# Performance work log

Hardware: AMD Instinct MI355X
Metric: run time of the kernel (lower is better)

## Reference

```python
import math
import jax, jax.numpy as jnp
import numpy as np

E = 1024      # embed_dim
K = 512       # key_dim
H = 16        # num_heads
W = 32        # scale window length (scale_lengths[0])
LENGTHS = [640, 512, 768, 384, 512, 576, 448, 256]
T = sum(LENGTHS)   # 4096 flat tokens
B = len(LENGTHS)
MAXL = max(LENGTHS)


def setup_inputs() -> dict:
    key = jax.random.key(0)
    ks = jax.random.split(key, 6)
    s = 0.02
    x = jax.random.normal(ks[0], (T, E), jnp.float32)
    Wkv = jax.random.normal(ks[1], (E + K, E), jnp.float32) * s
    bkv = jnp.zeros((E + K,), jnp.float32)
    Wq = jax.random.normal(ks[2], (K, E), jnp.float32) * s
    bq = jnp.zeros((K,), jnp.float32)
    Wp = jax.random.normal(ks[3], (E, E), jnp.float32) * s
    bp = jnp.zeros((E,), jnp.float32)
    # reset_parameters: init.uniform_ on layer buffer
    buffer = jax.random.uniform(ks[4], (W - 1, E + K), jnp.float32)
    sample_lengths = jnp.array(LENGTHS, jnp.int32)
    return {"x": x, "Wkv": Wkv, "bkv": bkv, "Wq": Wq, "bq": bq,
            "Wp": Wp, "bp": bp, "buffer": buffer,
            "sample_lengths": sample_lengths}


def reference(x, Wkv, bkv, Wq, bq, Wp, bp, buffer, sample_lengths):
    Tn, En = x.shape
    # per-token segment id and local position within the sample
    starts = jnp.concatenate([jnp.zeros((1,), sample_lengths.dtype),
                              jnp.cumsum(sample_lengths)[:-1]])
    t = jnp.arange(Tn, dtype=starts.dtype)
    seg = jnp.searchsorted(starts, t, side='right') - 1   # [T]
    j = t - starts[seg]                                   # local index in sample

    # key_value projection on the flat batch
    kv = x @ Wkv.T + bkv                                  # [T, E+K]

    # tile_within: window[c] = token(j - c) within sample, else learned buffer pad
    # (matches roll_by_gather semantics: window order is self, prev1, prev2, ...)
    c = jnp.arange(W)
    src = jnp.concatenate([buffer, kv], axis=0)           # [W-1 + T, E+K]
    data_idx = (W - 1) + t[:, None] - c[None, :]          # global token j - c
    buf_idx = (W - 1) + j[:, None] - c[None, :]           # buffer[W-1 + (j-c)]
    idx = jnp.where(j[:, None] >= c[None, :], data_idx, buf_idx)
    tiled = src[idx]                                      # [T, W, E+K]

    dk = K // H
    dv = En // H
    kh = tiled[..., :K].reshape(Tn, W, H, dk)
    vh = tiled[..., K:].reshape(Tn, W, H, dv)
    q = (x @ Wq.T + bq).reshape(Tn, H, dk)

    # single-query scaled dot-product attention over the W-window
    logits = jnp.einsum('thd,twhd->thw', q, kh) * (1.0 / math.sqrt(dk))
    p = jax.nn.softmax(logits, axis=-1)                   # [T, H, W]
    o = jnp.einsum('thw,twhd->thd', p, vh).reshape(Tn, En)
    out = o @ Wp.T + bp                                   # [T, E]

    # unflatten (pack/pad_sequence): scatter flat tokens into padded [B, MAXL, E]
    y = jnp.zeros((B, MAXL, En), out.dtype).at[seg, j].set(out)
    return y
```

## Files before the change

kernel.cpp:

```cpp
#include <hip/hip_runtime.h>

typedef __attribute__((ext_vector_type(8))) short short8v;
typedef __attribute__((ext_vector_type(4))) float f32x4;

__device__ inline unsigned short f2b(float f) {
    unsigned u = __builtin_bit_cast(unsigned, f);
    unsigned r = u + 0x7fffu + ((u >> 16) & 1u);
    return (unsigned short)(r >> 16);
}
__device__ inline void gload16(const void* g, void* l) {
    __builtin_amdgcn_global_load_lds(
        (const __attribute__((address_space(1))) void*)g,
        (__attribute__((address_space(3))) void*)l, 16, 0, 0);
}

__global__ __launch_bounds__(256)
void prep_kernel(const float* __restrict__ x, const float* __restrict__ wkv,
                 const float* __restrict__ wq, const float* __restrict__ wp,
                 const float* __restrict__ buf, const int* __restrict__ sl,
                 const float* __restrict__ bkv, const float* __restrict__ bq,
                 short* __restrict__ dst, short* __restrict__ ext,
                 int* __restrict__ extrow, int* __restrict__ destrow,
                 float* __restrict__ biascat,
                 long n0, long n1, long n2, long n3, long n4,
                 int T, int Bn, int MAXL, int EK, int NKVQ)
{
    long gid = (long)blockIdx.x * blockDim.x + threadIdx.x;
    long e = gid * 8;
    if (e < n3) {
        const float* s; long off;
        if (e < n0)      { s = x;   off = e; }
        else if (e < n1) { s = wkv; off = e - n0; }
        else if (e < n2) { s = wq;  off = e - n1; }
        else             { s = wp;  off = e - n2; }
        float4 a = *(const float4*)(s + off);
        float4 b = *(const float4*)(s + off + 4);
        short8v o;
        o[0] = (short)f2b(a.x); o[1] = (short)f2b(a.y);
        o[2] = (short)f2b(a.z); o[3] = (short)f2b(a.w);
        o[4] = (short)f2b(b.x); o[5] = (short)f2b(b.y);
        o[6] = (short)f2b(b.z); o[7] = (short)f2b(b.w);
        *(short8v*)(dst + e) = o;
    } else if (e < n4) {
        long off = e - n3;
        int brow = (int)(off / EK);
        int bcol = (int)(off % EK);
        float4 a = *(const float4*)(buf + off);
        float4 b = *(const float4*)(buf + off + 4);
        short8v o;
        o[0] = (short)f2b(a.x); o[1] = (short)f2b(a.y);
        o[2] = (short)f2b(a.z); o[3] = (short)f2b(a.w);
        o[4] = (short)f2b(b.x); o[5] = (short)f2b(b.y);
        o[6] = (short)f2b(b.z); o[7] = (short)f2b(b.w);
        int start = 0;
        for (int s = 0; s < 8; ++s) {
            int dr = 31 * s + start + brow;
            *(short8v*)&ext[(size_t)dr * EK + bcol] = o;
            start += sl[s];
        }
    }
    if (gid < T) {
        int start = 0, seg = 0, jloc = 0;
        for (int i = 0; i < Bn; ++i) {
            int len = sl[i];
            if (gid >= start && gid < start + len) { seg = i; jloc = (int)gid - start; }
            start += len;
        }
        destrow[gid] = seg * MAXL + jloc;
        extrow[gid]  = 31 * (seg + 1) + (int)gid;
    }
    if (gid < NKVQ) {
        biascat[gid] = (gid < EK) ? bkv[gid] : bq[gid - EK];
    }
}

__global__ __launch_bounds__(256)
void padzero_kernel(float* __restrict__ y, const int* __restrict__ sl,
                    int MAXL, int E)
{
    int row = blockIdx.x;
    int seg = row / MAXL, pos = row - seg * MAXL;
    if (pos < sl[seg]) return;
    float4 z = {0.f, 0.f, 0.f, 0.f};
    *(float4*)&y[(size_t)row * E + threadIdx.x * 4] = z;
}

template<int MODE>
__global__ __launch_bounds__(512)
void gemm8w(const short* __restrict__ A, const short* __restrict__ Bm,
            const float* __restrict__ bias,
            short* __restrict__ C0, short* __restrict__ C1,
            float* __restrict__ Cf, const int* __restrict__ rowmap,
            int M, int N, int Kd)
{
    __shared__ short lA[2][128 * 64];
    __shared__ short lB[2][128 * 64];
    int nb = N >> 7;
    int bid0 = blockIdx.x;
    int bid = (bid0 & 7) * ((int)gridDim.x >> 3) + (bid0 >> 3);
    int m0 = (bid / nb) << 7, n0 = (bid % nb) << 7;
    int tid = threadIdx.x;
    int lane = tid & 63, wid = tid >> 6;
    int wm = wid >> 1, wn = wid & 1;
    int nlo = lane & 15, g4 = lane >> 4;

    f32x4 acc[2][4];
    #pragma unroll
    for (int i = 0; i < 2; ++i)
        #pragma unroll
        for (int j2 = 0; j2 < 4; ++j2)
            acc[i][j2] = (f32x4)(0.f);

    int srow = tid >> 3;
    int scol = (tid & 7) * 8;
    const short* ga = A + (size_t)(m0 + srow) * Kd + scol;
    const short* gb = Bm + (size_t)(n0 + srow) * Kd + scol;

    auto stage = [&](int bf2, int k0) {
        gload16(ga + k0,                   &lA[bf2][srow * 64 + scol]);
        gload16(ga + (size_t)64 * Kd + k0, &lA[bf2][(64 + srow) * 64 + scol]);
        gload16(gb + k0,                   &lB[bf2][srow * 64 + scol]);
        gload16(gb + (size_t)64 * Kd + k0, &lB[bf2][(64 + srow) * 64 + scol]);
    };

    int nk = Kd >> 6;
    stage(0, 0);
    for (int t = 0; t < nk; ++t) {
        __syncthreads();
        if (t + 1 < nk) stage((t + 1) & 1, (t + 1) << 6);
        int cb = t & 1;
        #pragma unroll
        for (int ss = 0; ss < 2; ++ss) {
            short8v af[2], bf[4];
            #pragma unroll
            for (int f = 0; f < 2; ++f)
                af[f] = *(const short8v*)
                    &lA[cb][(wm * 32 + f * 16 + nlo) * 64 + ss * 32 + g4 * 8];
            #pragma unroll
            for (int f = 0; f < 4; ++f)
                bf[f] = *(const short8v*)
                    &lB[cb][(wn * 64 + f * 16 + nlo) * 64 + ss * 32 + g4 * 8];
            #pragma unroll
            for (int i = 0; i < 2; ++i)
                #pragma unroll
                for (int j2 = 0; j2 < 4; ++j2)
                    acc[i][j2] = __builtin_amdgcn_mfma_f32_16x16x32_bf16(
                        af[i], bf[j2], acc[i][j2], 0, 0, 0);
        }
    }

    int cr = g4 * 4;
    float bv[4];
    #pragma unroll
    for (int j2 = 0; j2 < 4; ++j2)
        bv[j2] = bias[n0 + wn * 64 + j2 * 16 + nlo];
    #pragma unroll
    for (int i = 0; i < 2; ++i) {
        #pragma unroll
        for (int rr = 0; rr < 4; ++rr) {
            int row = m0 + wm * 32 + i * 16 + cr + rr;
            int dr = rowmap[row];
            #pragma unroll
            for (int j2 = 0; j2 < 4; ++j2) {
                int col = n0 + wn * 64 + j2 * 16 + nlo;
                float v = acc[i][j2][rr] + bv[j2];
                if (MODE == 0) {
                    if (col < 1536)
                        C0[(size_t)dr * 1536 + col] = (short)f2b(v);
                    else
                        C1[(size_t)row * 512 + (col - 1536)] = (short)f2b(v);
                } else {
                    Cf[(size_t)dr * N + col] = v;
                }
            }
        }
    }
}

__global__ __launch_bounds__(256)
void attn6_kernel(const short* __restrict__ ext, const short* __restrict__ qb,
                  const int* __restrict__ extrow, short* __restrict__ o)
{
    __shared__ short lK[4 * 48 * 40];
    __shared__ short lV[4 * 48 * 66];
    __shared__ short ps[4 * 16 * 76];

    int bid = blockIdx.x;
    int swz = (bid & 7) * (gridDim.x >> 3) + (bid >> 3);
    int tg = swz >> 2, hg = swz & 3;
    int t0 = tg << 4, h0 = hg << 2;
    int r0 = extrow[t0] - 31;
    int tid = threadIdx.x;
    int wv = tid >> 6, lane = tid & 63;

    #pragma unroll
    for (int p = 0; p < 3; ++p) {
        int q = p * 256 + tid;
        int hd = q / 192;
        int rem = q - hd * 192;
        int rr = rem >> 2, cc = rem & 3;
        int sr = r0 + (rr < 47 ? rr : 46);
        *(short8v*)&lK[hd * 1920 + rr * 40 + cc * 8] =
            *(const short8v*)&ext[(size_t)sr * 1536 + (h0 + hd) * 32 + cc * 8];
    }
    #pragma unroll
    for (int p = 0; p < 6; ++p) {
        int q = p * 256 + tid;
        int hd = q / 384;
        int rem = q - hd * 384;
        int rr = rem >> 3, cc = rem & 7;
        int sr = r0 + (rr < 47 ? rr : 46);
        *(short8v*)&lV[hd * 3168 + rr * 66 + cc * 8] =
            *(const short8v*)&ext[(size_t)sr * 1536 + 512 + (h0 + hd) * 64 + cc * 8];
    }
    if (tid < 128) {
        int hd = tid >> 5, row = (tid >> 1) & 15, hf = tid & 1;
        uint4 z = {0u, 0u, 0u, 0u};
        *(uint4*)&ps[hd * 1216 + row * 76 + 48 + hf * 8] = z;
    }

    int h = h0 + wv;
    int nlo = lane & 15, g4 = lane >> 4;

    short8v aq = *(const short8v*)&qb[(size_t)(t0 + nlo) * 512 + h * 32 + g4 * 8];

    __syncthreads();

    f32x4 sg[3];
    #pragma unroll
    for (int g = 0; g < 3; ++g) {
        short8v bk = *(const short8v*)&lK[wv * 1920 + (g * 16 + nlo) * 40 + g4 * 8];
        f32x4 z = (f32x4)(0.f);
        sg[g] = __builtin_amdgcn_mfma_f32_16x16x32_bf16(aq, bk, z, 0, 0, 0);
    }

    const float scale = 0.17677669529663687f;
    #pragma unroll
    for (int r = 0; r < 4; ++r) {
        int tk = g4 * 4 + r;
        bool v0 = (nlo >= tk);
        bool v2 = (nlo < tk);
        float s0 = v0 ? sg[0][r] * scale : -1e30f;
        float s1 = sg[1][r] * scale;
        float s2 = v2 ? sg[2][r] * scale : -1e30f;
        float m = fmaxf(fmaxf(s0, s1), s2);
        m = fmaxf(m, __shfl_xor(m, 1, 64));
        m = fmaxf(m, __shfl_xor(m, 2, 64));
        m = fmaxf(m, __shfl_xor(m, 4, 64));
        m = fmaxf(m, __shfl_xor(m, 8, 64));
        float p0 = v0 ? __expf(s0 - m) : 0.f;
        float p1 = __expf(s1 - m);
        float p2 = v2 ? __expf(s2 - m) : 0.f;
        float sm = p0 + p1 + p2;
        sm += __shfl_xor(sm, 1, 64);
        sm += __shfl_xor(sm, 2, 64);
        sm += __shfl_xor(sm, 4, 64);
        sm += __shfl_xor(sm, 8, 64);
        float inv = 1.f / sm;
        short* pr = &ps[wv * 1216 + tk * 76];
        pr[nlo]      = (short)f2b(p0 * inv);
        pr[16 + nlo] = (short)f2b(p1 * inv);
        pr[32 + nlo] = (short)f2b(p2 * inv);
    }

    short8v pa0 = *(const short8v*)&ps[wv * 1216 + nlo * 76 + g4 * 8];
    short8v pa1 = *(const short8v*)&ps[wv * 1216 + nlo * 76 + 32 + g4 * 8];
    #pragma unroll
    for (int dvt = 0; dvt < 4; ++dvt) {
        f32x4 acc = (f32x4)(0.f);
        short8v b0, b1;
        #pragma unroll
        for (int j = 0; j < 8; ++j) {
            int lr = g4 * 8 + j;
            b0[j] = lV[wv * 3168 + lr * 66 + dvt * 16 + nlo];
        }
        acc = __builtin_amdgcn_mfma_f32_16x16x32_bf16(pa0, b0, acc, 0, 0, 0);
        #pragma unroll
        for (int j = 0; j < 8; ++j) {
            int lr = 32 + g4 * 8 + j;
            int rowc = lr < 47 ? lr : 47;
            b1[j] = lV[wv * 3168 + rowc * 66 + dvt * 16 + nlo];
        }
        acc = __builtin_amdgcn_mfma_f32_16x16x32_bf16(pa1, b1, acc, 0, 0, 0);
        #pragma unroll
        for (int r = 0; r < 4; ++r) {
            int t = t0 + g4 * 4 + r;
            o[(size_t)t * 1024 + h * 64 + dvt * 16 + nlo] = (short)f2b(acc[r]);
        }
    }
}

extern "C" void kernel_launch(void* const* d_in, const int* in_sizes, int n_in,
                              void* d_out, int out_size, void* d_ws, size_t ws_size,
                              hipStream_t stream)
{
    const float* x      = (const float*)d_in[0];
    const float* Wkv    = (const float*)d_in[1];
    const float* bkv    = (const float*)d_in[2];
    const float* Wq     = (const float*)d_in[3];
    const float* bq     = (const float*)d_in[4];
    const float* Wp     = (const float*)d_in[5];
    const float* bp     = (const float*)d_in[6];
    const float* buffer = (const float*)d_in[7];
    const int*   sl     = (const int*)d_in[8];

    int E  = in_sizes[6];
    int Kc = in_sizes[4];
    int T  = in_sizes[0] / E;
    int Bn = in_sizes[8];
    int EK = E + Kc;
    int NKVQ = EK + Kc;
    int MAXL = out_size / (Bn * E);
    int TEXT = T + 31 * Bn;

    size_t nX = (size_t)T * E, nWkv = (size_t)EK * E, nWq = (size_t)Kc * E;
    size_t nWp = (size_t)E * E, nBuf = (size_t)in_sizes[7];

    short* xb    = (short*)d_ws;
    short* wkvqb = xb + nX;
    short* wpb   = wkvqb + nWkv + nWq;
    short* qbuf  = wpb + nWp;
    short* extb  = qbuf + (size_t)T * Kc;
    short* ob    = extb + (size_t)TEXT * EK;
    int*   extrowp = (int*)(ob + (size_t)T * E);
    int*   destrow = extrowp + T;
    float* biascat = (float*)(destrow + T);

    float* y = (float*)d_out;

    long n0 = (long)nX, n1 = n0 + (long)nWkv, n2 = n1 + (long)nWq;
    long n3 = n2 + (long)nWp, n4 = n3 + (long)nBuf;
    int prep_blocks = (int)((n4 / 8 + 255) / 256);
    prep_kernel<<<prep_blocks, 256, 0, stream>>>(
        x, Wkv, Wq, Wp, buffer, sl, bkv, bq, xb, extb,
        extrowp, destrow, biascat,
        n0, n1, n2, n3, n4, T, Bn, MAXL, EK, NKVQ);

    padzero_kernel<<<Bn * MAXL, E / 4, 0, stream>>>(y, sl, MAXL, E);

    gemm8w<0><<<(T / 128) * (NKVQ / 128), 512, 0, stream>>>(
        xb, wkvqb, biascat, extb, qbuf, nullptr, extrowp, T, NKVQ, E);

    attn6_kernel<<<(T / 16) * 4, 256, 0, stream>>>(extb, qbuf, extrowp, ob);

    gemm8w<1><<<(T / 128) * (E / 128), 512, 0, stream>>>(
        ob, wpb, bp, nullptr, nullptr, y, destrow, T, E, E);
}
```

Baseline: 82.69 us.

## Fuse all stages into one persistent kernel with grid-wide barriers

Replaces the five separate launches (prep, pad-zero, QKV GEMM, window attention, output GEMM) with a single persistent kernel of 512 blocks of 256 threads. The stages are separated by an atomic grid barrier, and each block loops over several work tiles. GEMM tiles are re-shaped to K-step 32, and each block handles two attention tiles. The aim is to remove launch gaps and tail effects between kernels. In exchange it depends on all 512 blocks being co-resident, adds barrier spin cost, and lowers per-block thread counts for the GEMMs.

```diff
diff --git a/kernel.cpp b/kernel.cpp
--- a/kernel.cpp
+++ b/kernel.cpp
@@ -14,278 +14,324 @@
         (__attribute__((address_space(3))) void*)l, 16, 0, 0);
 }
 
-__global__ __launch_bounds__(256)
-void prep_kernel(const float* __restrict__ x, const float* __restrict__ wkv,
-                 const float* __restrict__ wq, const float* __restrict__ wp,
-                 const float* __restrict__ buf, const int* __restrict__ sl,
-                 const float* __restrict__ bkv, const float* __restrict__ bq,
-                 short* __restrict__ dst, short* __restrict__ ext,
-                 int* __restrict__ extrow, int* __restrict__ destrow,
-                 float* __restrict__ biascat,
-                 long n0, long n1, long n2, long n3, long n4,
-                 int T, int Bn, int MAXL, int EK, int NKVQ)
+__device__ __forceinline__ void gsync(int* cnt, int* gen) {
+    __syncthreads();
+    if (threadIdx.x == 0) {
+        int g = __hip_atomic_load(gen, __ATOMIC_ACQUIRE, __HIP_MEMORY_SCOPE_AGENT);
+        __threadfence();
+        int a = __hip_atomic_fetch_add(cnt, 1, __ATOMIC_ACQ_REL, __HIP_MEMORY_SCOPE_AGENT);
+        if (a == (int)gridDim.x - 1) {
+            __hip_atomic_store(cnt, 0, __ATOMIC_RELAXED, __HIP_MEMORY_SCOPE_AGENT);
+            __hip_atomic_fetch_add(gen, 1, __ATOMIC_RELEASE, __HIP_MEMORY_SCOPE_AGENT);
+        } else {
+            while (__hip_atomic_load(gen, __ATOMIC_ACQUIRE, __HIP_MEMORY_SCOPE_AGENT) == g)
+                __builtin_amdgcn_s_sleep(2);
+        }
+    }
+    __syncthreads();
+}
+
+__global__ __launch_bounds__(256, 2)
+void fused_kernel(const float* __restrict__ x, const float* __restrict__ wkv,
+                  const float* __restrict__ wq, const float* __restrict__ wp,
+                  const float* __restrict__ buf, const int* __restrict__ sl,
+                  const float* __restrict__ bkv, const float* __restrict__ bq,
+                  const float* __restrict__ bp,
+                  short* __restrict__ xb, short* __restrict__ wkvqb,
+                  short* __restrict__ wpb, short* __restrict__ qbuf,
+                  short* __restrict__ extb, short* __restrict__ ob,
+                  int* __restrict__ extrow, int* __restrict__ destrow,
+                  float* __restrict__ biascat, float* __restrict__ y,
+                  int* bar_cnt, int* bar_gen,
+                  long n0, long n1, long n2, long n3, long n4,
+                  int T, int Bn, int MAXL, int EK, int NKVQ)
 {
-    long gid = (long)blockIdx.x * blockDim.x + threadIdx.x;
-    long e = gid * 8;
-    if (e < n3) {
-        const float* s; long off;
-        if (e < n0)      { s = x;   off = e; }
-        else if (e < n1) { s = wkv; off = e - n0; }
-        else if (e < n2) { s = wq;  off = e - n1; }
-        else             { s = wp;  off = e - n2; }
-        float4 a = *(const float4*)(s + off);
-        float4 b = *(const float4*)(s + off + 4);
-        short8v o;
-        o[0] = (short)f2b(a.x); o[1] = (short)f2b(a.y);
-        o[2] = (short)f2b(a.z); o[3] = (short)f2b(a.w);
-        o[4] = (short)f2b(b.x); o[5] = (short)f2b(b.y);
-        o[6] = (short)f2b(b.z); o[7] = (short)f2b(b.w);
-        *(short8v*)(dst + e) = o;
-    } else if (e < n4) {
-        long off = e - n3;
-        int brow = (int)(off / EK);
-        int bcol = (int)(off % EK);
-        float4 a = *(const float4*)(buf + off);
-        float4 b = *(const float4*)(buf + off + 4);
-        short8v o;
-        o[0] = (short)f2b(a.x); o[1] = (short)f2b(a.y);
-        o[2] = (short)f2b(a.z); o[3] = (short)f2b(a.w);
-        o[4] = (short)f2b(b.x); o[5] = (short)f2b(b.y);
-        o[6] = (short)f2b(b.z); o[7] = (short)f2b(b.w);
-        int start = 0;
-        for (int s = 0; s < 8; ++s) {
-            int dr = 31 * s + start + brow;
-            *(short8v*)&ext[(size_t)dr * EK + bcol] = o;
-            start += sl[s];
-        }
-    }
-    if (gid < T) {
-        int start = 0, seg = 0, jloc = 0;
-        for (int i = 0; i < Bn; ++i) {
-            int len = sl[i];
-            if (gid >= start && gid < start + len) { seg = i; jloc = (int)gid - start; }
-            start += len;
-        }
-        destrow[gid] = seg * MAXL + jloc;
-        extrow[gid]  = 31 * (seg + 1) + (int)gid;
-    }
-    if (gid < NKVQ) {
-        biascat[gid] = (gid < EK) ? bkv[gid] : bq[gid - EK];
-    }
-}
-
-__global__ __launch_bounds__(256)
-void padzero_kernel(float* __restrict__ y, const int* __restrict__ sl,
-                    int MAXL, int E)
-{
-    int row = blockIdx.x;
-    int seg = row / MAXL, pos = row - seg * MAXL;
-    if (pos < sl[seg]) return;
-    float4 z = {0.f, 0.f, 0.f, 0.f};
-    *(float4*)&y[(size_t)row * E + threadIdx.x * 4] = z;
-}
-
-template<int MODE>
-__global__ __launch_bounds__(512)
-void gemm8w(const short* __restrict__ A, const short* __restrict__ Bm,
-            const float* __restrict__ bias,
-            short* __restrict__ C0, short* __restrict__ C1,
-            float* __restrict__ Cf, const int* __restrict__ rowmap,
-            int M, int N, int Kd)
-{
-    __shared__ short lA[2][128 * 64];
-    __shared__ short lB[2][128 * 64];
-    int nb = N >> 7;
-    int bid0 = blockIdx.x;
-    int bid = (bid0 & 7) * ((int)gridDim.x >> 3) + (bid0 >> 3);
-    int m0 = (bid / nb) << 7, n0 = (bid % nb) << 7;
-    int tid = threadIdx.x;
-    int lane = tid & 63, wid = tid >> 6;
-    int wm = wid >> 1, wn = wid & 1;
-    int nlo = lane & 15, g4 = lane >> 4;
-
-    f32x4 acc[2][4];
-    #pragma unroll
-    for (int i = 0; i < 2; ++i)
-        #pragma unroll
-        for (int j2 = 0; j2 < 4; ++j2)
-            acc[i][j2] = (f32x4)(0.f);
-
-    int srow = tid >> 3;
-    int scol = (tid & 7) * 8;
-    const short* ga = A + (size_t)(m0 + srow) * Kd + scol;
-    const short* gb = Bm + (size_t)(n0 + srow) * Kd + scol;
-
-    auto stage = [&](int bf2, int k0) {
-        gload16(ga + k0,                   &lA[bf2][srow * 64 + scol]);
-        gload16(ga + (size_t)64 * Kd + k0, &lA[bf2][(64 + srow) * 64 + scol]);
-        gload16(gb + k0,                   &lB[bf2][srow * 64 + scol]);
-        gload16(gb + (size_t)64 * Kd + k0, &lB[bf2][(64 + srow) * 64 + scol]);
-    };
-
-    int nk = Kd >> 6;
-    stage(0, 0);
-    for (int t = 0; t < nk; ++t) {
-        __syncthreads();
-        if (t + 1 < nk) stage((t + 1) & 1, (t + 1) << 6);
-        int cb = t & 1;
-        #pragma unroll
-        for (int ss = 0; ss < 2; ++ss) {
-            short8v af[2], bf[4];
-            #pragma unroll
-            for (int f = 0; f < 2; ++f)
-                af[f] = *(const short8v*)
-                    &lA[cb][(wm * 32 + f * 16 + nlo) * 64 + ss * 32 + g4 * 8];
+    __shared__ __align__(16) char pool[50432];
+    const int tid = threadIdx.x;
+    const int lane = tid & 63, wid = tid >> 6;
+    const int nlo = lane & 15, g4 = lane >> 4;
+
+    {
+        long gs = (long)gridDim.x * blockDim.x;
+        long gid0 = (long)blockIdx.x * blockDim.x + tid;
+        for (long e = gid0 * 8; e < n4; e += gs * 8) {
+            if (e < n3) {
+                const float* s; long off;
+                if (e < n0)      { s = x;   off = e; }
+                else if (e < n1) { s = wkv; off = e - n0; }
+                else if (e < n2) { s = wq;  off = e - n1; }
+                else             { s = wp;  off = e - n2; }
+                float4 a = *(const float4*)(s + off);
+                float4 b = *(const float4*)(s + off + 4);
+                short8v o;
+                o[0] = (short)f2b(a.x); o[1] = (short)f2b(a.y);
+                o[2] = (short)f2b(a.z); o[3] = (short)f2b(a.w);
+                o[4] = (short)f2b(b.x); o[5] = (short)f2b(b.y);
+                o[6] = (short)f2b(b.z); o[7] = (short)f2b(b.w);
+                *(short8v*)(xb + e) = o;
+            } else {
+                long off = e - n3;
+                int brow = (int)(off / EK);
+                int bcol = (int)(off % EK);
+                float4 a = *(const float4*)(buf + off);
+                float4 b = *(const float4*)(buf + off + 4);
+                short8v o;
+                o[0] = (short)f2b(a.x); o[1] = (short)f2b(a.y);
+                o[2] = (short)f2b(a.z); o[3] = (short)f2b(a.w);
+                o[4] = (short)f2b(b.x); o[5] = (short)f2b(b.y);
+                o[6] = (short)f2b(b.z); o[7] = (short)f2b(b.w);
+                int start = 0;
+                for (int s8 = 0; s8 < Bn; ++s8) {
+                    int dr = 31 * s8 + start + brow;
+                    *(short8v*)&extb[(size_t)dr * EK + bcol] = o;
+                    start += sl[s8];
+                }
+            }
+        }
+        if (gid0 < T) {
+            int start = 0, seg = 0, jloc = 0;
+            for (int i = 0; i < Bn; ++i) {
+                int len = sl[i];
+                if (gid0 >= start && gid0 < start + len) { seg = i; jloc = (int)gid0 - start; }
+                start += len;
+            }
+            destrow[gid0] = seg * MAXL + jloc;
+            extrow[gid0]  = 31 * (seg + 1) + (int)gid0;
+        }
+        if (gid0 < NKVQ)
+            biascat[gid0] = (gid0 < EK) ? bkv[gid0] : bq[gid0 - EK];
+        for (int row = blockIdx.x; row < Bn * MAXL; row += gridDim.x) {
+            int seg = row / MAXL, pos = row - seg * MAXL;
+            if (pos >= sl[seg]) {
+                float4 z = {0.f, 0.f, 0.f, 0.f};
+                *(float4*)&y[(size_t)row * 1024 + tid * 4] = z;
+            }
+        }
+    }
+    gsync(bar_cnt, bar_gen);
+
+    {
+        short* lA = (short*)pool;
+        short* lB = (short*)(pool + 16384);
+        int bid = (blockIdx.x & 7) * 64 + (blockIdx.x >> 3);
+        int m0 = (bid >> 4) << 7, nn0 = (bid & 15) << 7;
+        int wm = wid >> 1, wn = wid & 1;
+        f32x4 acc[4][4];
+        #pragma unroll
+        for (int i = 0; i < 4; ++i)
+            #pragma unroll
+            for (int j2 = 0; j2 < 4; ++j2)
+                acc[i][j2] = (f32x4)(0.f);
+        int srow = tid >> 2, scol = (tid & 3) * 8;
+        const short* ga = xb + (size_t)(m0 + srow) * 1024 + scol;
+        const short* gb = wkvqb + (size_t)(nn0 + srow) * 1024 + scol;
+        auto stage1 = [&](int b2, int k0) {
+            gload16(ga + k0,           &lA[b2 * 4096 + tid * 8]);
+            gload16(ga + 65536 + k0,   &lA[b2 * 4096 + 2048 + tid * 8]);
+            gload16(gb + k0,           &lB[b2 * 4096 + tid * 8]);
+            gload16(gb + 65536 + k0,   &lB[b2 * 4096 + 2048 + tid * 8]);
+        };
+        stage1(0, 0);
+        for (int t = 0; t < 32; ++t) {
+            __syncthreads();
+            if (t + 1 < 32) stage1((t + 1) & 1, (t + 1) << 5);
+            int cb = t & 1;
+            short8v af[4], bf[4];
             #pragma unroll
             for (int f = 0; f < 4; ++f)
-                bf[f] = *(const short8v*)
-                    &lB[cb][(wn * 64 + f * 16 + nlo) * 64 + ss * 32 + g4 * 8];
-            #pragma unroll
-            for (int i = 0; i < 2; ++i)
+                af[f] = *(const short8v*)&lA[cb * 4096 + (wm * 64 + f * 16 + nlo) * 32 + g4 * 8];
+            #pragma unroll
+            for (int f = 0; f < 4; ++f)
+                bf[f] = *(const short8v*)&lB[cb * 4096 + (wn * 64 + f * 16 + nlo) * 32 + g4 * 8];
+            #pragma unroll
+            for (int i = 0; i < 4; ++i)
                 #pragma unroll
                 for (int j2 = 0; j2 < 4; ++j2)
                     acc[i][j2] = __builtin_amdgcn_mfma_f32_16x16x32_bf16(
                         af[i], bf[j2], acc[i][j2], 0, 0, 0);
         }
-    }
-
-    int cr = g4 * 4;
-    float bv[4];
-    #pragma unroll
-    for (int j2 = 0; j2 < 4; ++j2)
-        bv[j2] = bias[n0 + wn * 64 + j2 * 16 + nlo];
-    #pragma unroll
-    for (int i = 0; i < 2; ++i) {
-        #pragma unroll
-        for (int rr = 0; rr < 4; ++rr) {
-            int row = m0 + wm * 32 + i * 16 + cr + rr;
-            int dr = rowmap[row];
-            #pragma unroll
-            for (int j2 = 0; j2 < 4; ++j2) {
-                int col = n0 + wn * 64 + j2 * 16 + nlo;
-                float v = acc[i][j2][rr] + bv[j2];
-                if (MODE == 0) {
+        int cr = g4 * 4;
+        float bv[4];
+        #pragma unroll
+        for (int j2 = 0; j2 < 4; ++j2)
+            bv[j2] = biascat[nn0 + wn * 64 + j2 * 16 + nlo];
+        #pragma unroll
+        for (int i = 0; i < 4; ++i) {
+            #pragma unroll
+            for (int rr = 0; rr < 4; ++rr) {
+                int row = m0 + wm * 64 + i * 16 + cr + rr;
+                int dr = extrow[row];
+                #pragma unroll
+                for (int j2 = 0; j2 < 4; ++j2) {
+                    int col = nn0 + wn * 64 + j2 * 16 + nlo;
+                    float v = acc[i][j2][rr] + bv[j2];
                     if (col < 1536)
-                        C0[(size_t)dr * 1536 + col] = (short)f2b(v);
+                        extb[(size_t)dr * 1536 + col] = (short)f2b(v);
                     else
-                        C1[(size_t)row * 512 + (col - 1536)] = (short)f2b(v);
-                } else {
-                    Cf[(size_t)dr * N + col] = v;
-                }
-            }
-        }
-    }
-}
-
-__global__ __launch_bounds__(256)
-void attn6_kernel(const short* __restrict__ ext, const short* __restrict__ qb,
-                  const int* __restrict__ extrow, short* __restrict__ o)
-{
-    __shared__ short lK[4 * 48 * 40];
-    __shared__ short lV[4 * 48 * 66];
-    __shared__ short ps[4 * 16 * 76];
-
-    int bid = blockIdx.x;
-    int swz = (bid & 7) * (gridDim.x >> 3) + (bid >> 3);
-    int tg = swz >> 2, hg = swz & 3;
-    int t0 = tg << 4, h0 = hg << 2;
-    int r0 = extrow[t0] - 31;
-    int tid = threadIdx.x;
-    int wv = tid >> 6, lane = tid & 63;
-
-    #pragma unroll
-    for (int p = 0; p < 3; ++p) {
-        int q = p * 256 + tid;
-        int hd = q / 192;
-        int rem = q - hd * 192;
-        int rr = rem >> 2, cc = rem & 3;
-        int sr = r0 + (rr < 47 ? rr : 46);
-        *(short8v*)&lK[hd * 1920 + rr * 40 + cc * 8] =
-            *(const short8v*)&ext[(size_t)sr * 1536 + (h0 + hd) * 32 + cc * 8];
-    }
-    #pragma unroll
-    for (int p = 0; p < 6; ++p) {
-        int q = p * 256 + tid;
-        int hd = q / 384;
-        int rem = q - hd * 384;
-        int rr = rem >> 3, cc = rem & 7;
-        int sr = r0 + (rr < 47 ? rr : 46);
-        *(short8v*)&lV[hd * 3168 + rr * 66 + cc * 8] =
-            *(const short8v*)&ext[(size_t)sr * 1536 + 512 + (h0 + hd) * 64 + cc * 8];
-    }
-    if (tid < 128) {
-        int hd = tid >> 5, row = (tid >> 1) & 15, hf = tid & 1;
-        uint4 z = {0u, 0u, 0u, 0u};
-        *(uint4*)&ps[hd * 1216 + row * 76 + 48 + hf * 8] = z;
-    }
-
-    int h = h0 + wv;
-    int nlo = lane & 15, g4 = lane >> 4;
-
-    short8v aq = *(const short8v*)&qb[(size_t)(t0 + nlo) * 512 + h * 32 + g4 * 8];
-
-    __syncthreads();
-
-    f32x4 sg[3];
-    #pragma unroll
-    for (int g = 0; g < 3; ++g) {
-        short8v bk = *(const short8v*)&lK[wv * 1920 + (g * 16 + nlo) * 40 + g4 * 8];
-        f32x4 z = (f32x4)(0.f);
-        sg[g] = __builtin_amdgcn_mfma_f32_16x16x32_bf16(aq, bk, z, 0, 0, 0);
-    }
-
-    const float scale = 0.17677669529663687f;
-    #pragma unroll
-    for (int r = 0; r < 4; ++r) {
-        int tk = g4 * 4 + r;
-        bool v0 = (nlo >= tk);
-        bool v2 = (nlo < tk);
-        float s0 = v0 ? sg[0][r] * scale : -1e30f;
-        float s1 = sg[1][r] * scale;
-        float s2 = v2 ? sg[2][r] * scale : -1e30f;
-        float m = fmaxf(fmaxf(s0, s1), s2);
-        m = fmaxf(m, __shfl_xor(m, 1, 64));
-        m = fmaxf(m, __shfl_xor(m, 2, 64));
-        m = fmaxf(m, __shfl_xor(m, 4, 64));
-        m = fmaxf(m, __shfl_xor(m, 8, 64));
-        float p0 = v0 ? __expf(s0 - m) : 0.f;
-        float p1 = __expf(s1 - m);
-        float p2 = v2 ? __expf(s2 - m) : 0.f;
-        float sm = p0 + p1 + p2;
-        sm += __shfl_xor(sm, 1, 64);
-        sm += __shfl_xor(sm, 2, 64);
-        sm += __shfl_xor(sm, 4, 64);
-        sm += __shfl_xor(sm, 8, 64);
-        float inv = 1.f / sm;
-        short* pr = &ps[wv * 1216 + tk * 76];
-        pr[nlo]      = (short)f2b(p0 * inv);
-        pr[16 + nlo] = (short)f2b(p1 * inv);
-        pr[32 + nlo] = (short)f2b(p2 * inv);
-    }
-
-    short8v pa0 = *(const short8v*)&ps[wv * 1216 + nlo * 76 + g4 * 8];
-    short8v pa1 = *(const short8v*)&ps[wv * 1216 + nlo * 76 + 32 + g4 * 8];
-    #pragma unroll
-    for (int dvt = 0; dvt < 4; ++dvt) {
-        f32x4 acc = (f32x4)(0.f);
-        short8v b0, b1;
-        #pragma unroll
-        for (int j = 0; j < 8; ++j) {
-            int lr = g4 * 8 + j;
-            b0[j] = lV[wv * 3168 + lr * 66 + dvt * 16 + nlo];
-        }
-        acc = __builtin_amdgcn_mfma_f32_16x16x32_bf16(pa0, b0, acc, 0, 0, 0);
-        #pragma unroll
-        for (int j = 0; j < 8; ++j) {
-            int lr = 32 + g4 * 8 + j;
-            int rowc = lr < 47 ? lr : 47;
-            b1[j] = lV[wv * 3168 + rowc * 66 + dvt * 16 + nlo];
-        }
-        acc = __builtin_amdgcn_mfma_f32_16x16x32_bf16(pa1, b1, acc, 0, 0, 0);
-        #pragma unroll
-        for (int r = 0; r < 4; ++r) {
-            int t = t0 + g4 * 4 + r;
-            o[(size_t)t * 1024 + h * 64 + dvt * 16 + nlo] = (short)f2b(acc[r]);
+                        qbuf[(size_t)row * 512 + (col - 1536)] = (short)f2b(v);
+                }
+            }
+        }
+    }
+    gsync(bar_cnt, bar_gen);
+
+    {
+        short* lK = (short*)pool;
+        short* lV = (short*)(pool + 15360);
+        short* ps = (short*)(pool + 40704);
+        int sb = (blockIdx.x & 7) * 64 + (blockIdx.x >> 3);
+        if (tid < 128) {
+            int hd = tid >> 5, rw = (tid >> 1) & 15, hf = tid & 1;
+            uint4 z = {0u, 0u, 0u, 0u};
+            *(uint4*)&ps[hd * 1216 + rw * 76 + 48 + hf * 8] = z;
+        }
+        #pragma unroll 1
+        for (int it = 0; it < 2; ++it) {
+            int tile = sb * 2 + it;
+            int tg = tile >> 2, hg = tile & 3;
+            int t0 = tg << 4, h0 = hg << 2;
+            int r0 = extrow[t0] - 31;
+            if (it) __syncthreads();
+            #pragma unroll
+            for (int p = 0; p < 3; ++p) {
+                int q = p * 256 + tid;
+                int hd = q / 192, rem = q - hd * 192;
+                int rr = rem >> 2, cc = rem & 3;
+                int sr = r0 + (rr < 47 ? rr : 46);
+                *(short8v*)&lK[hd * 1920 + rr * 40 + cc * 8] =
+                    *(const short8v*)&extb[(size_t)sr * 1536 + (h0 + hd) * 32 + cc * 8];
+            }
+            #pragma unroll
+            for (int p = 0; p < 6; ++p) {
+                int q = p * 256 + tid;
+                int hd = q / 384, rem = q - hd * 384;
+                int rr = rem >> 3, cc = rem & 7;
+                int sr = r0 + (rr < 47 ? rr : 46);
+                *(short8v*)&lV[hd * 3168 + rr * 66 + cc * 8] =
+                    *(const short8v*)&extb[(size_t)sr * 1536 + 512 + (h0 + hd) * 64 + cc * 8];
+            }
+            int h = h0 + wid;
+            short8v aq = *(const short8v*)&qbuf[(size_t)(t0 + nlo) * 512 + h * 32 + g4 * 8];
+            __syncthreads();
+            f32x4 sg[3];
+            #pragma unroll
+            for (int g = 0; g < 3; ++g) {
+                short8v bk = *(const short8v*)&lK[wid * 1920 + (g * 16 + nlo) * 40 + g4 * 8];
+                f32x4 z = (f32x4)(0.f);
+                sg[g] = __builtin_amdgcn_mfma_f32_16x16x32_bf16(aq, bk, z, 0, 0, 0);
+            }
+            const float scale = 0.17677669529663687f;
+            #pragma unroll
+            for (int r = 0; r < 4; ++r) {
+                int tk = g4 * 4 + r;
+                bool v0 = (nlo >= tk);
+                bool v2 = (nlo < tk);
+                float s0 = v0 ? sg[0][r] * scale : -1e30f;
+                float s1 = sg[1][r] * scale;
+                float s2 = v2 ? sg[2][r] * scale : -1e30f;
+                float m = fmaxf(fmaxf(s0, s1), s2);
+                m = fmaxf(m, __shfl_xor(m, 1, 64));
+                m = fmaxf(m, __shfl_xor(m, 2, 64));
+                m = fmaxf(m, __shfl_xor(m, 4, 64));
+                m = fmaxf(m, __shfl_xor(m, 8, 64));
+                float p0 = v0 ? __expf(s0 - m) : 0.f;
+                float p1 = __expf(s1 - m);
+                float p2 = v2 ? __expf(s2 - m) : 0.f;
+                float sm = p0 + p1 + p2;
+                sm += __shfl_xor(sm, 1, 64);
+                sm += __shfl_xor(sm, 2, 64);
+                sm += __shfl_xor(sm, 4, 64);
+                sm += __shfl_xor(sm, 8, 64);
+                float inv = 1.f / sm;
+                short* pr = &ps[wid * 1216 + tk * 76];
+                pr[nlo]      = (short)f2b(p0 * inv);
+                pr[16 + nlo] = (short)f2b(p1 * inv);
+                pr[32 + nlo] = (short)f2b(p2 * inv);
+            }
+            short8v pa0 = *(const short8v*)&ps[wid * 1216 + nlo * 76 + g4 * 8];
+            short8v pa1 = *(const short8v*)&ps[wid * 1216 + nlo * 76 + 32 + g4 * 8];
+            #pragma unroll
+            for (int dvt = 0; dvt < 4; ++dvt) {
+                f32x4 acc = (f32x4)(0.f);
+                short8v b0, b1;
+                #pragma unroll
+                for (int j = 0; j < 8; ++j)
+                    b0[j] = lV[wid * 3168 + (g4 * 8 + j) * 66 + dvt * 16 + nlo];
+                acc = __builtin_amdgcn_mfma_f32_16x16x32_bf16(pa0, b0, acc, 0, 0, 0);
+                #pragma unroll
+                for (int j = 0; j < 8; ++j) {
+                    int lr = 32 + g4 * 8 + j;
+                    int rowc = lr < 47 ? lr : 47;
+                    b1[j] = lV[wid * 3168 + rowc * 66 + dvt * 16 + nlo];
+                }
+                acc = __builtin_amdgcn_mfma_f32_16x16x32_bf16(pa1, b1, acc, 0, 0, 0);
+                #pragma unroll
+                for (int r = 0; r < 4; ++r) {
+                    int t = t0 + g4 * 4 + r;
+                    ob[(size_t)t * 1024 + h * 64 + dvt * 16 + nlo] = (short)f2b(acc[r]);
+                }
+            }
+        }
+    }
+    gsync(bar_cnt, bar_gen);
+
+    {
+        short* lA = (short*)pool;
+        short* lB = (short*)(pool + 8192);
+        int bid = (blockIdx.x & 7) * 64 + (blockIdx.x >> 3);
+        int m0 = (bid >> 3) * 64, nn0 = (bid & 7) << 7;
+        int wm = wid >> 1, wn = wid & 1;
+        f32x4 acc[2][4];
+        #pragma unroll
+        for (int i = 0; i < 2; ++i)
+            #pragma unroll
+            for (int j2 = 0; j2 < 4; ++j2)
+                acc[i][j2] = (f32x4)(0.f);
+        int srow = tid >> 2, scol = (tid & 3) * 8;
+        const short* ga = ob + (size_t)(m0 + srow) * 1024 + scol;
+        const short* gb = wpb + (size_t)(nn0 + srow) * 1024 + scol;
+        auto stage2 = [&](int b2, int k0) {
+            if (srow < 64)
+                gload16(ga + k0, &lA[b2 * 2048 + tid * 8]);
+            gload16(gb + k0,         &lB[b2 * 4096 + tid * 8]);
+            gload16(gb + 65536 + k0, &lB[b2 * 4096 + 2048 + tid * 8]);
+        };
+        stage2(0, 0);
+        for (int t = 0; t < 32; ++t) {
+            __syncthreads();
+            if (t + 1 < 32) stage2((t + 1) & 1, (t + 1) << 5);
+            int cb = t & 1;
+            short8v af[2], bf[4];
+            #pragma unroll
+            for (int f = 0; f < 2; ++f)
+                af[f] = *(const short8v*)&lA[cb * 2048 + (wm * 32 + f * 16 + nlo) * 32 + g4 * 8];
+            #pragma unroll
+            for (int f = 0; f < 4; ++f)
+                bf[f] = *(const short8v*)&lB[cb * 4096 + (wn * 64 + f * 16 + nlo) * 32 + g4 * 8];
+            #pragma unroll
+            for (int i = 0; i < 2; ++i)
+                #pragma unroll
+                for (int j2 = 0; j2 < 4; ++j2)
+                    acc[i][j2] = __builtin_amdgcn_mfma_f32_16x16x32_bf16(
+                        af[i], bf[j2], acc[i][j2], 0, 0, 0);
+        }
+        int cr = g4 * 4;
+        float bv[4];
+        #pragma unroll
+        for (int j2 = 0; j2 < 4; ++j2)
+            bv[j2] = bp[nn0 + wn * 64 + j2 * 16 + nlo];
+        #pragma unroll
+        for (int i = 0; i < 2; ++i) {
+            #pragma unroll
+            for (int rr = 0; rr < 4; ++rr) {
+                int row = m0 + wm * 32 + i * 16 + cr + rr;
+                int dr = destrow[row];
+                #pragma unroll
+                for (int j2 = 0; j2 < 4; ++j2) {
+                    int col = nn0 + wn * 64 + j2 * 16 + nlo;
+                    y[(size_t)dr * 1024 + col] = acc[i][j2][rr] + bv[j2];
+                }
+            }
         }
     }
 }
@@ -325,24 +371,17 @@
     int*   extrowp = (int*)(ob + (size_t)T * E);
     int*   destrow = extrowp + T;
     float* biascat = (float*)(destrow + T);
+    int*   barp    = (int*)(biascat + NKVQ);
 
     float* y = (float*)d_out;
 
     long n0 = (long)nX, n1 = n0 + (long)nWkv, n2 = n1 + (long)nWq;
     long n3 = n2 + (long)nWp, n4 = n3 + (long)nBuf;
-    int prep_blocks = (int)((n4 / 8 + 255) / 256);
-    prep_kernel<<<prep_blocks, 256, 0, stream>>>(
-        x, Wkv, Wq, Wp, buffer, sl, bkv, bq, xb, extb,
-        extrowp, destrow, biascat,
+
+    hipMemsetAsync(barp, 0, 2 * sizeof(int), stream);
+    fused_kernel<<<512, 256, 0, stream>>>(
+        x, Wkv, Wq, Wp, buffer, sl, bkv, bq, bp,
+        xb, wkvqb, wpb, qbuf, extb, ob,
+        extrowp, destrow, biascat, y, barp, barp + 1,
         n0, n1, n2, n3, n4, T, Bn, MAXL, EK, NKVQ);
-
-    padzero_kernel<<<Bn * MAXL, E / 4, 0, stream>>>(y, sl, MAXL, E);
-
-    gemm8w<0><<<(T / 128) * (NKVQ / 128), 512, 0, stream>>>(
-        xb, wkvqb, biascat, extb, qbuf, nullptr, extrowp, T, NKVQ, E);
-
-    attn6_kernel<<<(T / 16) * 4, 256, 0, stream>>>(extb, qbuf, extrowp, ob);
-
-    gemm8w<1><<<(T / 128) * (E / 128), 512, 0, stream>>>(
-        ob, wpb, bp, nullptr, nullptr, y, destrow, T, E, E);
-}
+}
```

Result: slower. 274.2 us (+231.6%).

## Use 64x128 four-wave GEMM tiles and fold pad zeroing into prep kernel

Applied to the files above, without the earlier changes.

Both GEMMs move from 128x128 eight-wave blocks with a K-step of 64 to 64x128 four-wave blocks with a K-step of 32. This doubles the block count so more of the CUs are kept busy, and it shrinks LDS use per block. The separate padzero launch is merged into the prep kernel, which is now launched with one block per padded output row, removing one kernel launch. In exchange, each tile gets less operand reuse, each block runs twice as many K iterations and barriers, and the prep grid is oversized for the conversion work.

```diff
diff --git a/kernel.cpp b/kernel.cpp
--- a/kernel.cpp
+++ b/kernel.cpp
@@ -21,7 +21,7 @@
                  const float* __restrict__ bkv, const float* __restrict__ bq,
                  short* __restrict__ dst, short* __restrict__ ext,
                  int* __restrict__ extrow, int* __restrict__ destrow,
-                 float* __restrict__ biascat,
+                 float* __restrict__ biascat, float* __restrict__ y,
                  long n0, long n1, long n2, long n3, long n4,
                  int T, int Bn, int MAXL, int EK, int NKVQ)
 {
@@ -53,10 +53,10 @@
         o[4] = (short)f2b(b.x); o[5] = (short)f2b(b.y);
         o[6] = (short)f2b(b.z); o[7] = (short)f2b(b.w);
         int start = 0;
-        for (int s = 0; s < 8; ++s) {
-            int dr = 31 * s + start + brow;
+        for (int s8 = 0; s8 < 8; ++s8) {
+            int dr = 31 * s8 + start + brow;
             *(short8v*)&ext[(size_t)dr * EK + bcol] = o;
-            start += sl[s];
+            start += sl[s8];
         }
     }
     if (gid < T) {
@@ -72,33 +72,30 @@
     if (gid < NKVQ) {
         biascat[gid] = (gid < EK) ? bkv[gid] : bq[gid - EK];
     }
-}
-
+    int row = blockIdx.x;
+    if (row < Bn * MAXL) {
+        int seg = row / MAXL, pos = row - seg * MAXL;
+        if (pos >= sl[seg]) {
+            float4 z = {0.f, 0.f, 0.f, 0.f};
+            *(float4*)&y[(size_t)row * 1024 + threadIdx.x * 4] = z;
+        }
+    }
+}
+
+template<int MODE>
 __global__ __launch_bounds__(256)
-void padzero_kernel(float* __restrict__ y, const int* __restrict__ sl,
-                    int MAXL, int E)
+void gemm64t(const short* __restrict__ A, const short* __restrict__ Bm,
+             const float* __restrict__ bias,
+             short* __restrict__ C0, short* __restrict__ C1,
+             float* __restrict__ Cf, const int* __restrict__ rowmap,
+             int M, int N, int Kd)
 {
-    int row = blockIdx.x;
-    int seg = row / MAXL, pos = row - seg * MAXL;
-    if (pos < sl[seg]) return;
-    float4 z = {0.f, 0.f, 0.f, 0.f};
-    *(float4*)&y[(size_t)row * E + threadIdx.x * 4] = z;
-}
-
-template<int MODE>
-__global__ __launch_bounds__(512)
-void gemm8w(const short* __restrict__ A, const short* __restrict__ Bm,
-            const float* __restrict__ bias,
-            short* __restrict__ C0, short* __restrict__ C1,
-            float* __restrict__ Cf, const int* __restrict__ rowmap,
-            int M, int N, int Kd)
-{
-    __shared__ short lA[2][128 * 64];
-    __shared__ short lB[2][128 * 64];
+    __shared__ short lA[2][64 * 32];
+    __shared__ short lB[2][128 * 32];
     int nb = N >> 7;
     int bid0 = blockIdx.x;
     int bid = (bid0 & 7) * ((int)gridDim.x >> 3) + (bid0 >> 3);
-    int m0 = (bid / nb) << 7, n0 = (bid % nb) << 7;
+    int m0 = (bid / nb) << 6, n0 = (bid % nb) << 7;
     int tid = threadIdx.x;
     int lane = tid & 63, wid = tid >> 6;
     int wm = wid >> 1, wn = wid & 1;
@@ -111,42 +108,36 @@
         for (int j2 = 0; j2 < 4; ++j2)
             acc[i][j2] = (f32x4)(0.f);
 
-    int srow = tid >> 3;
-    int scol = (tid & 7) * 8;
+    const int srow = tid >> 2;
+    const int scol = (tid & 3) * 8;
     const short* ga = A + (size_t)(m0 + srow) * Kd + scol;
     const short* gb = Bm + (size_t)(n0 + srow) * Kd + scol;
 
     auto stage = [&](int bf2, int k0) {
-        gload16(ga + k0,                   &lA[bf2][srow * 64 + scol]);
-        gload16(ga + (size_t)64 * Kd + k0, &lA[bf2][(64 + srow) * 64 + scol]);
-        gload16(gb + k0,                   &lB[bf2][srow * 64 + scol]);
-        gload16(gb + (size_t)64 * Kd + k0, &lB[bf2][(64 + srow) * 64 + scol]);
+        gload16(ga + k0, &lA[bf2][tid * 8]);
+        gload16(gb + k0, &lB[bf2][tid * 8]);
+        gload16(gb + (size_t)64 * Kd + k0, &lB[bf2][64 * 32 + tid * 8]);
     };
 
-    int nk = Kd >> 6;
+    int nk = Kd >> 5;
     stage(0, 0);
     for (int t = 0; t < nk; ++t) {
         __syncthreads();
-        if (t + 1 < nk) stage((t + 1) & 1, (t + 1) << 6);
+        if (t + 1 < nk) stage((t + 1) & 1, (t + 1) << 5);
         int cb = t & 1;
-        #pragma unroll
-        for (int ss = 0; ss < 2; ++ss) {
-            short8v af[2], bf[4];
+        short8v af[2], bf[4];
+        #pragma unroll
+        for (int f = 0; f < 2; ++f)
+            af[f] = *(const short8v*)&lA[cb][(wm * 32 + f * 16 + nlo) * 32 + g4 * 8];
+        #pragma unroll
+        for (int f = 0; f < 4; ++f)
+            bf[f] = *(const short8v*)&lB[cb][(wn * 64 + f * 16 + nlo) * 32 + g4 * 8];
+        #pragma unroll
+        for (int i = 0; i < 2; ++i)
             #pragma unroll
-            for (int f = 0; f < 2; ++f)
-                af[f] = *(const short8v*)
-                    &lA[cb][(wm * 32 + f * 16 + nlo) * 64 + ss * 32 + g4 * 8];
-            #pragma unroll
-            for (int f = 0; f < 4; ++f)
-                bf[f] = *(const short8v*)
-                    &lB[cb][(wn * 64 + f * 16 + nlo) * 64 + ss * 32 + g4 * 8];
-            #pragma unroll
-            for (int i = 0; i < 2; ++i)
-                #pragma unroll
-                for (int j2 = 0; j2 < 4; ++j2)
-                    acc[i][j2] = __builtin_amdgcn_mfma_f32_16x16x32_bf16(
-                        af[i], bf[j2], acc[i][j2], 0, 0, 0);
-        }
+            for (int j2 = 0; j2 < 4; ++j2)
+                acc[i][j2] = __builtin_amdgcn_mfma_f32_16x16x32_bf16(
+                    af[i], bf[j2], acc[i][j2], 0, 0, 0);
     }
 
     int cr = g4 * 4;
@@ -196,8 +187,7 @@
     #pragma unroll
     for (int p = 0; p < 3; ++p) {
         int q = p * 256 + tid;
-        int hd = q / 192;
-        int rem = q - hd * 192;
+        int hd = q / 192, rem = q - hd * 192;
         int rr = rem >> 2, cc = rem & 3;
         int sr = r0 + (rr < 47 ? rr : 46);
         *(short8v*)&lK[hd * 1920 + rr * 40 + cc * 8] =
@@ -206,8 +196,7 @@
     #pragma unroll
     for (int p = 0; p < 6; ++p) {
         int q = p * 256 + tid;
-        int hd = q / 384;
-        int rem = q - hd * 384;
+        int hd = q / 384, rem = q - hd * 384;
         int rr = rem >> 3, cc = rem & 7;
         int sr = r0 + (rr < 47 ? rr : 46);
         *(short8v*)&lV[hd * 3168 + rr * 66 + cc * 8] =
@@ -270,10 +259,8 @@
         f32x4 acc = (f32x4)(0.f);
         short8v b0, b1;
         #pragma unroll
-        for (int j = 0; j < 8; ++j) {
-            int lr = g4 * 8 + j;
-            b0[j] = lV[wv * 3168 + lr * 66 + dvt * 16 + nlo];
-        }
+        for (int j = 0; j < 8; ++j)
+            b0[j] = lV[wv * 3168 + (g4 * 8 + j) * 66 + dvt * 16 + nlo];
         acc = __builtin_amdgcn_mfma_f32_16x16x32_bf16(pa0, b0, acc, 0, 0, 0);
         #pragma unroll
         for (int j = 0; j < 8; ++j) {
@@ -330,19 +317,17 @@
 
     long n0 = (long)nX, n1 = n0 + (long)nWkv, n2 = n1 + (long)nWq;
     long n3 = n2 + (long)nWp, n4 = n3 + (long)nBuf;
-    int prep_blocks = (int)((n4 / 8 + 255) / 256);
+    int prep_blocks = Bn * MAXL;
     prep_kernel<<<prep_blocks, 256, 0, stream>>>(
         x, Wkv, Wq, Wp, buffer, sl, bkv, bq, xb, extb,
-        extrowp, destrow, biascat,
+        extrowp, destrow, biascat, y,
         n0, n1, n2, n3, n4, T, Bn, MAXL, EK, NKVQ);
 
-    padzero_kernel<<<Bn * MAXL, E / 4, 0, stream>>>(y, sl, MAXL, E);
-
-    gemm8w<0><<<(T / 128) * (NKVQ / 128), 512, 0, stream>>>(
+    gemm64t<0><<<(T / 64) * (NKVQ / 128), 256, 0, stream>>>(
         xb, wkvqb, biascat, extb, qbuf, nullptr, extrowp, T, NKVQ, E);
 
     attn6_kernel<<<(T / 16) * 4, 256, 0, stream>>>(extb, qbuf, extrowp, ob);
 
-    gemm8w<1><<<(T / 128) * (E / 128), 512, 0, stream>>>(
+    gemm64t<1><<<(T / 64) * (E / 128), 256, 0, stream>>>(
         ob, wpb, bp, nullptr, nullptr, y, destrow, T, E, E);
 }
```

Result: faster. 69.92 us (median of 4 runs) (-15.4%).
